# Kernel optimization log

Measured on AMD Instinct MI355X. Metric: run time of the kernel, lower is better.

The kernel has to match this reference:

```python
import jax, jax.numpy as jnp
import numpy as np
import math

D_MODEL, N_HEADS, D_FF = 512, 8, 2048
B, S = 4, 2048
EPS = 1e-6


def _layernorm(x, alpha, bias):
    # Faithful to the torch module: std is unbiased (ddof=1) and eps is added to std, not var.
    m = jnp.mean(x, axis=-1, keepdims=True)
    s = jnp.std(x, axis=-1, keepdims=True, ddof=1)
    return alpha * (x - m) / (s + EPS) + bias


def setup_inputs() -> dict:
    key = jax.random.key(0)
    ks = jax.random.split(key, 16)
    d, f = D_MODEL, D_FF
    sd = 1.0 / math.sqrt(d)
    sf = 1.0 / math.sqrt(f)
    return {
        "x": jax.random.normal(ks[0], (B, S, d), jnp.float32),
        "wq": jax.random.normal(ks[1], (d, d), jnp.float32) * sd,
        "bq": jnp.zeros((d,), jnp.float32),
        "wk": jax.random.normal(ks[2], (d, d), jnp.float32) * sd,
        "bk": jnp.zeros((d,), jnp.float32),
        "wv": jax.random.normal(ks[3], (d, d), jnp.float32) * sd,
        "bv": jnp.zeros((d,), jnp.float32),
        "wo": jax.random.normal(ks[4], (d, d), jnp.float32) * sd,
        "bo": jnp.zeros((d,), jnp.float32),
        "w1": jax.random.normal(ks[5], (d, f), jnp.float32) * sd,
        "b1": jnp.zeros((f,), jnp.float32),
        "w2": jax.random.normal(ks[6], (f, d), jnp.float32) * sf,
        "b2": jnp.zeros((d,), jnp.float32),
        "ln1_a": jnp.ones((d,), jnp.float32),
        "ln1_b": jnp.zeros((d,), jnp.float32),
        "ln2_a": jnp.ones((d,), jnp.float32),
        "ln2_b": jnp.zeros((d,), jnp.float32),
    }


def reference(x, wq, bq, wk, bk, wv, bv, wo, bo, w1, b1, w2, b2, ln1_a, ln1_b, ln2_a, ln2_b):
    b, s, d = x.shape
    h, dk = N_HEADS, d // N_HEADS
    # QKV projections -> [b, h, s, dk]
    q = (x @ wq + bq).reshape(b, s, h, dk).transpose(0, 2, 1, 3)
    k = (x @ wk + bk).reshape(b, s, h, dk).transpose(0, 2, 1, 3)
    v = (x @ wv + bv).reshape(b, s, h, dk).transpose(0, 2, 1, 3)
    # Manual scaled-dot-product attention (no mask in EncoderBlock path)
    scores = jnp.einsum("bhqd,bhkd->bhqk", q, k) / jnp.sqrt(jnp.float32(dk))
    probs = jax.nn.softmax(scores, axis=-1)
    attn = jnp.einsum("bhqk,bhkd->bhqd", probs, v)
    concat = attn.transpose(0, 2, 1, 3).reshape(b, s, d)
    mha_out = concat @ wo + bo
    # Residual + LayerNorm 1
    y = _layernorm(x + mha_out, ln1_a, ln1_b)
    # FFN + Residual + LayerNorm 2
    ff = jax.nn.relu(y @ w1 + b1) @ w2 + b2
    return _layernorm(y + ff, ln2_a, ln2_b)
```

## Files before the change

kernel.cpp:

```cpp
#include <hip/hip_runtime.h>
#include <hip/hip_bf16.h>


typedef __bf16 bf16;
typedef __bf16 bf16x4 __attribute__((ext_vector_type(4)));
typedef __bf16 bf16x8 __attribute__((ext_vector_type(8)));
typedef float  f32x4  __attribute__((ext_vector_type(4)));

#define NBATCH 4
#define SEQ    2048
#define DMODEL 512
#define NHEADS 8
#define DHEAD  64
#define DFF    2048
#define MTOT   (NBATCH * SEQ)
#define WS_NEED 73940992u

__device__ __forceinline__ f32x4 mfma16(bf16x8 a, bf16x8 b, f32x4 c) {
    return __builtin_amdgcn_mfma_f32_16x16x32_bf16(a, b, c, 0, 0, 0);
}

__device__ __forceinline__ void lds16(const bf16* g, bf16* l) {
    __builtin_amdgcn_global_load_lds(
        (const __attribute__((address_space(1))) void*)g,
        (__attribute__((address_space(3))) void*)l, 16, 0, 0);
}

__device__ __forceinline__ float scrub(float f) {
    return (fabsf(f) < 1e30f) ? f : 0.f;
}

__global__ void sentinel_kernel(bf16* out) {
    out[threadIdx.x] = (bf16)1000.0f;
}

__global__ __launch_bounds__(256) void prep_kernel(
        const float* x,
        const float* wq, const float* wk, const float* wv, const float* wo,
        const float* w1, const float* w2,
        const float* bq, const float* bk, const float* bv, const float* bo,
        const float* b1, const float* b2,
        const float* l1a, const float* l1b, const float* l2a, const float* l2b,
        bf16* __restrict__ xcv,
        bf16* __restrict__ wT, bf16* __restrict__ w1T, bf16* __restrict__ w2T,
        bf16* __restrict__ prm) {
    __shared__ bf16 tile[32][33];
    int b = blockIdx.x;
    if (b < 4096) {
        int i = (b * 256 + threadIdx.x) * 4;
        float4 f = *(const float4*)(x + i);
        bf16x4 o = {(bf16)scrub(f.x), (bf16)scrub(f.y),
                    (bf16)scrub(f.z), (bf16)scrub(f.w)};
        *(bf16x4*)(xcv + i) = o;
        return;
    }
    if (b < 4106) {
        int pb = b - 4096;
        const float* srcs[10] = {bq, bk, bv, bo, b1, b2, l1a, l1b, l2a, l2b};
        const int len[10] = {512,512,512,512,2048,512,512,512,512,512};
        const int dst[10] = {0,512,1024,1536,2048,4096,4608,5120,5632,6144};
        const float* s = srcs[pb];
        bf16* d = prm + dst[pb];
        for (int i = threadIdx.x; i < len[pb]; i += 256)
            d[i] = (bf16)scrub(s[i]);
        return;
    }
    const float* in; bf16* out; int K, N, bx, by;
    if (b < 5130) {
        int idx = b - 4106, z = idx >> 8, rem = idx & 255;
        const float* srcs[4] = {wq, wk, wv, wo};
        in = srcs[z]; out = wT + (size_t)z * 262144;
        K = 512; N = 512; bx = rem & 15; by = rem >> 4;
    } else if (b < 6154) {
        int idx = b - 5130;
        in = w1; out = w1T; K = 512; N = 2048; bx = idx & 63; by = idx >> 6;
    } else {
        int idx = b - 6154;
        in = w2; out = w2T; K = 2048; N = 512; bx = idx & 15; by = idx >> 4;
    }
    int tx = threadIdx.x & 31, ty = threadIdx.x >> 5;
    int n0 = bx * 32, k0 = by * 32;
#pragma unroll
    for (int i = 0; i < 4; i++) {
        int kl = ty * 4 + i;
        tile[kl][tx] = (bf16)scrub(in[(size_t)(k0 + kl) * N + n0 + tx]);
    }
    __syncthreads();
#pragma unroll
    for (int i = 0; i < 4; i++) {
        int nl = ty * 4 + i;
        out[(size_t)(n0 + nl) * K + k0 + tx] = tile[tx][nl];
    }
}

template <bool RELU>
__global__ __launch_bounds__(256) void gemm_bt(
        const bf16* __restrict__ A, const bf16* __restrict__ BT,
        const bf16* __restrict__ bias, bf16* __restrict__ Cout,
        int M, int N, int K) {
    constexpr int BM = 128, BN = 128, BK = 32;
    __shared__ __align__(16) bf16 As[BM * BK];
    __shared__ __align__(16) bf16 Bs[BN * BK];

    int tid  = threadIdx.x;
    int wid  = tid >> 6, lane = tid & 63;
    int quad = lane >> 4, l15 = lane & 15;
    int mb = blockIdx.x * BM, nb = blockIdx.y * BN;
    int wm = (wid >> 1) * 64, wn = (wid & 1) * 64;

    f32x4 acc[4][4] = {};

    int c0 = wid * 128 + lane, c1 = c0 + 64;
    int ar0 = c0 >> 2, ac0 = (c0 & 3) * 8;
    int ar1 = c1 >> 2, ac1 = (c1 & 3) * 8;
    bf16* lA0 = &As[(wid * 2 + 0) * 512];
    bf16* lA1 = &As[(wid * 2 + 1) * 512];
    bf16* lB0 = &Bs[(wid * 2 + 0) * 512];
    bf16* lB1 = &Bs[(wid * 2 + 1) * 512];

    for (int k0 = 0; k0 < K; k0 += BK) {
        __syncthreads();
        lds16(&A [(size_t)(mb + ar0) * K + k0 + ac0], lA0);
        lds16(&A [(size_t)(mb + ar1) * K + k0 + ac1], lA1);
        lds16(&BT[(size_t)(nb + ar0) * K + k0 + ac0], lB0);
        lds16(&BT[(size_t)(nb + ar1) * K + k0 + ac1], lB1);
        __syncthreads();

        bf16x8 af[4], bfr[4];
#pragma unroll
        for (int i = 0; i < 4; i++)
            af[i] = *(const bf16x8*)&As[(wm + i * 16 + l15) * 32 + quad * 8];
#pragma unroll
        for (int j = 0; j < 4; j++)
            bfr[j] = *(const bf16x8*)&Bs[(wn + j * 16 + l15) * 32 + quad * 8];
#pragma unroll
        for (int i = 0; i < 4; i++)
#pragma unroll
            for (int j = 0; j < 4; j++)
                acc[i][j] = mfma16(af[i], bfr[j], acc[i][j]);
    }

#pragma unroll
    for (int j = 0; j < 4; j++) {
        int n = nb + wn + j * 16 + l15;
        float bv = (float)bias[n];
#pragma unroll
        for (int i = 0; i < 4; i++) {
            int mBase = mb + wm + i * 16 + quad * 4;
#pragma unroll
            for (int r = 0; r < 4; r++) {
                float v = acc[i][j][r] + bv;
                if (RELU) v = v > 0.f ? v : 0.f;
                Cout[(size_t)(mBase + r) * N + n] = (bf16)v;
            }
        }
    }
}

template <bool RELU>
__global__ __launch_bounds__(256) void gemm_bt64(
        const bf16* __restrict__ A, const bf16* __restrict__ BT,
        const bf16* __restrict__ bias, bf16* __restrict__ Cout,
        int M, int N, int K) {
    constexpr int BM = 64, BN = 128;
    __shared__ __align__(16) bf16 As0[BM * 32], As1[BM * 32];
    __shared__ __align__(16) bf16 Bs0[BN * 32], Bs1[BN * 32];

    int tid  = threadIdx.x;
    int wid  = tid >> 6, lane = tid & 63;
    int quad = lane >> 4, l15 = lane & 15;
    int mb = blockIdx.x * BM, nb = blockIdx.y * BN;
    int wm = (wid >> 1) * 32, wn = (wid & 1) * 64;

    f32x4 acc[2][4] = {};

    int cA = wid * 64 + lane;
    int arA = cA >> 2, acA = (cA & 3) * 8;
    int cB0 = wid * 128 + lane, cB1 = cB0 + 64;
    int br0 = cB0 >> 2, bc0 = (cB0 & 3) * 8;
    int br1 = cB1 >> 2, bc1 = (cB1 & 3) * 8;
    bf16* lA0  = &As0[wid * 512];
    bf16* lA1  = &As1[wid * 512];
    bf16* lB00 = &Bs0[wid * 1024];
    bf16* lB01 = &Bs0[wid * 1024 + 512];
    bf16* lB10 = &Bs1[wid * 1024];
    bf16* lB11 = &Bs1[wid * 1024 + 512];

    for (int k0 = 0; k0 < K; k0 += 64) {
        __syncthreads();
        lds16(&A [(size_t)(mb + arA) * K + k0 + acA],      lA0);
        lds16(&A [(size_t)(mb + arA) * K + k0 + 32 + acA], lA1);
        lds16(&BT[(size_t)(nb + br0) * K + k0 + bc0],      lB00);
        lds16(&BT[(size_t)(nb + br1) * K + k0 + bc1],      lB01);
        lds16(&BT[(size_t)(nb + br0) * K + k0 + 32 + bc0], lB10);
        lds16(&BT[(size_t)(nb + br1) * K + k0 + 32 + bc1], lB11);
        __syncthreads();

        bf16x8 a0[2], a1[2], b0[4], b1[4];
#pragma unroll
        for (int i = 0; i < 2; i++) {
            a0[i] = *(const bf16x8*)&As0[(wm + i * 16 + l15) * 32 + quad * 8];
            a1[i] = *(const bf16x8*)&As1[(wm + i * 16 + l15) * 32 + quad * 8];
        }
#pragma unroll
        for (int j = 0; j < 4; j++) {
            b0[j] = *(const bf16x8*)&Bs0[(wn + j * 16 + l15) * 32 + quad * 8];
            b1[j] = *(const bf16x8*)&Bs1[(wn + j * 16 + l15) * 32 + quad * 8];
        }
#pragma unroll
        for (int i = 0; i < 2; i++)
#pragma unroll
            for (int j = 0; j < 4; j++)
                acc[i][j] = mfma16(a1[i], b1[j], mfma16(a0[i], b0[j], acc[i][j]));
    }

#pragma unroll
    for (int j = 0; j < 4; j++) {
        int n = nb + wn + j * 16 + l15;
        float bv = (float)bias[n];
#pragma unroll
        for (int i = 0; i < 2; i++) {
            int mBase = mb + wm + i * 16 + quad * 4;
#pragma unroll
            for (int r = 0; r < 4; r++) {
                float v = acc[i][j][r] + bv;
                if (RELU) v = v > 0.f ? v : 0.f;
                Cout[(size_t)(mBase + r) * N + n] = (bf16)v;
            }
        }
    }
}

__global__ __launch_bounds__(256) void gemm_qkv(
        const bf16* __restrict__ A, const bf16* __restrict__ BT,
        const bf16* __restrict__ bias,
        bf16* __restrict__ Cq, bf16* __restrict__ Ck, bf16* __restrict__ Cv,
        int M, int N, int K) {
    constexpr int BM = 128, BN = 128, BK = 32;
    __shared__ __align__(16) bf16 As[BM * BK];
    __shared__ __align__(16) bf16 Bs[BN * BK];
    __shared__ __align__(16) bf16 Ts[128 * 136];

    int tid  = threadIdx.x;
    int wid  = tid >> 6, lane = tid & 63;
    int quad = lane >> 4, l15 = lane & 15;
    int mb = blockIdx.x * BM, nb = blockIdx.y * BN;
    int wm = (wid >> 1) * 64, wn = (wid & 1) * 64;

    f32x4 acc[4][4] = {};

    int c0 = wid * 128 + lane, c1 = c0 + 64;
    int ar0 = c0 >> 2, ac0 = (c0 & 3) * 8;
    int ar1 = c1 >> 2, ac1 = (c1 & 3) * 8;
    bf16* lA0 = &As[(wid * 2 + 0) * 512];
    bf16* lA1 = &As[(wid * 2 + 1) * 512];
    bf16* lB0 = &Bs[(wid * 2 + 0) * 512];
    bf16* lB1 = &Bs[(wid * 2 + 1) * 512];

    for (int k0 = 0; k0 < K; k0 += BK) {
        __syncthreads();
        lds16(&A [(size_t)(mb + ar0) * K + k0 + ac0], lA0);
        lds16(&A [(size_t)(mb + ar1) * K + k0 + ac1], lA1);
        lds16(&BT[(size_t)(nb + ar0) * K + k0 + ac0], lB0);
        lds16(&BT[(size_t)(nb + ar1) * K + k0 + ac1], lB1);
        __syncthreads();

        bf16x8 af[4], bfr[4];
#pragma unroll
        for (int i = 0; i < 4; i++)
            af[i] = *(const bf16x8*)&As[(wm + i * 16 + l15) * 32 + quad * 8];
#pragma unroll
        for (int j = 0; j < 4; j++)
            bfr[j] = *(const bf16x8*)&Bs[(wn + j * 16 + l15) * 32 + quad * 8];
#pragma unroll
        for (int i = 0; i < 4; i++)
#pragma unroll
            for (int j = 0; j < 4; j++)
                acc[i][j] = mfma16(af[i], bfr[j], acc[i][j]);
    }

    int reg = nb >> 9;
    if (reg < 2) {
        bf16* C = reg ? Ck : Cq;
        float scl = reg ? 1.0f : 0.125f;
#pragma unroll
        for (int j = 0; j < 4; j++) {
            int n = nb + wn + j * 16 + l15;
            float bv = (float)bias[n];
            int nn = n & 511;
            int h = nn >> 6, dk = nn & 63;
#pragma unroll
            for (int i = 0; i < 4; i++) {
                int mBase = mb + wm + i * 16 + quad * 4;
#pragma unroll
                for (int r = 0; r < 4; r++) {
                    float v = (acc[i][j][r] + bv) * scl;
                    int m = mBase + r;
                    int b = m >> 11, s = m & (SEQ - 1);
                    C[((size_t)(b * NHEADS + h) * SEQ + s) * DHEAD + dk] = (bf16)v;
                }
            }
        }
    } else {
#pragma unroll
        for (int j = 0; j < 4; j++) {
            int nl = wn + j * 16 + l15;
            float bv = (float)bias[nb + nl];
#pragma unroll
            for (int i = 0; i < 4; i++) {
                int ml = wm + i * 16 + quad * 4;
                bf16x4 pk;
#pragma unroll
                for (int r = 0; r < 4; r++) pk[r] = (bf16)(acc[i][j][r] + bv);
                *(bf16x4*)&Ts[nl * 136 + ml] = pk;
            }
        }
        __syncthreads();
        int nl = tid >> 1, half = tid & 1;
        int nn = (nb + nl) & 511;
        int h = nn >> 6, dk = nn & 63;
        int bb = mb >> 11, s0 = mb & (SEQ - 1);
        bf16* dst = &Cv[((size_t)(bb * NHEADS + h) * DHEAD + dk) * SEQ + s0 + half * 64];
        const bf16* srcl = &Ts[nl * 136 + half * 64];
#pragma unroll
        for (int v = 0; v < 8; v++)
            *(uint4*)(dst + v * 8) = *(const uint4*)(srcl + v * 8);
    }
}

__global__ __launch_bounds__(256) void attn_kernel(
        const bf16* __restrict__ Q, const bf16* __restrict__ K,
        const bf16* __restrict__ VT,
        float* __restrict__ Opart, float* __restrict__ lpart) {
    __shared__ __align__(16) bf16 Ks[2][64 * 72];
    __shared__ __align__(16) bf16 Vs[2][64 * 72];
    __shared__ __align__(16) bf16 Pb[4][16 * 72];
    int tid  = threadIdx.x;
    int wid  = tid >> 6, lane = tid & 63;
    int quad = lane >> 4, l15 = lane & 15;
    int bh = blockIdx.y;
    int z  = blockIdx.z;
    int qb = blockIdx.x * 128 + wid * 32;
    int kb0 = z * (SEQ / 2);

    const bf16* Qh = Q  + (size_t)bh * SEQ * DHEAD;
    const bf16* Kh = K  + (size_t)bh * SEQ * DHEAD;
    const bf16* Vh = VT + (size_t)bh * DHEAD * SEQ;

    bf16x8 bQ0[2], bQ1[2];
#pragma unroll
    for (int c = 0; c < 2; c++) {
        const bf16* qp = &Qh[(qb + c * 16 + l15) * DHEAD + quad * 8];
        bQ0[c] = *(const bf16x8*)qp;
        bQ1[c] = *(const bf16x8*)(qp + 32);
    }

    int cc0 = tid * 2, cc1 = cc0 + 1;
    int kr0 = cc0 >> 3, kc0 = (cc0 & 7) * 8;
    int kr1 = cc1 >> 3, kc1 = (cc1 & 7) * 8;

    float lrow[2] = {0.f, 0.f};
    f32x4 Oacc[2][4] = {};

    {
        uint4 ka0 = *(const uint4*)&Kh[(size_t)(kb0 + kr0) * DHEAD + kc0];
        uint4 ka1 = *(const uint4*)&Kh[(size_t)(kb0 + kr1) * DHEAD + kc1];
        uint4 va0 = *(const uint4*)&Vh[(size_t)kr0 * SEQ + kb0 + kc0];
        uint4 va1 = *(const uint4*)&Vh[(size_t)kr1 * SEQ + kb0 + kc1];
        *(uint4*)&Ks[0][kr0 * 72 + kc0] = ka0;
        *(uint4*)&Ks[0][kr1 * 72 + kc1] = ka1;
        *(uint4*)&Vs[0][kr0 * 72 + kc0] = va0;
        *(uint4*)&Vs[0][kr1 * 72 + kc1] = va1;
    }
    __syncthreads();

    for (int it = 0; it < 16; it++) {
        int cur = it & 1, nxt = cur ^ 1;
        int kb = kb0 + (it + 1) * 64;
        uint4 nk0, nk1, nv0, nv1;
        bool pf = (it + 1 < 16);
        if (pf) {
            nk0 = *(const uint4*)&Kh[(size_t)(kb + kr0) * DHEAD + kc0];
            nk1 = *(const uint4*)&Kh[(size_t)(kb + kr1) * DHEAD + kc1];
            nv0 = *(const uint4*)&Vh[(size_t)kr0 * SEQ + kb + kc0];
            nv1 = *(const uint4*)&Vh[(size_t)kr1 * SEQ + kb + kc1];
        }

        bf16x8 aK0[4], aK1[4], bV0[4], bV1[4];
#pragma unroll
        for (int t = 0; t < 4; t++) {
            const bf16* kp = &Ks[cur][(t * 16 + l15) * 72 + quad * 8];
            aK0[t] = *(const bf16x8*)kp;
            aK1[t] = *(const bf16x8*)(kp + 32);
            const bf16* vp = &Vs[cur][(t * 16 + l15) * 72 + quad * 8];
            bV0[t] = *(const bf16x8*)vp;
            bV1[t] = *(const bf16x8*)(vp + 32);
        }

#pragma unroll
        for (int c = 0; c < 2; c++) {
            f32x4 st[4];
#pragma unroll
            for (int t = 0; t < 4; t++) {
                f32x4 zv = {0.f, 0.f, 0.f, 0.f};
                st[t] = mfma16(aK1[t], bQ1[c], mfma16(aK0[t], bQ0[c], zv));
            }
            bf16* myP = Pb[wid];
#pragma unroll
            for (int t = 0; t < 4; t++) {
                bf16x4 pk;
                float ps = 0.f;
#pragma unroll
                for (int r = 0; r < 4; r++) {
                    float p = __expf(fminf(st[t][r], 60.f));
                    ps += p;
                    pk[r] = (bf16)p;
                }
                lrow[c] += ps;
                *(bf16x4*)&myP[l15 * 72 + t * 16 + quad * 4] = pk;
            }
            bf16x8 aP0 = *(const bf16x8*)&myP[l15 * 72 + quad * 8];
            bf16x8 aP1 = *(const bf16x8*)&myP[l15 * 72 + 32 + quad * 8];
#pragma unroll
            for (int nt = 0; nt < 4; nt++)
                Oacc[c][nt] = mfma16(aP1, bV1[nt],
                                     mfma16(aP0, bV0[nt], Oacc[c][nt]));
        }

        if (pf) {
            *(uint4*)&Ks[nxt][kr0 * 72 + kc0] = nk0;
            *(uint4*)&Ks[nxt][kr1 * 72 + kc1] = nk1;
            *(uint4*)&Vs[nxt][kr0 * 72 + kc0] = nv0;
            *(uint4*)&Vs[nxt][kr1 * 72 + kc1] = nv1;
        }
        __syncthreads();
    }

    int b = bh >> 3, hd = bh & 7;
    float* Op = Opart + (size_t)z * (MTOT * (size_t)DMODEL);
#pragma unroll
    for (int c = 0; c < 2; c++) {
        float l = lrow[c];
        l += __shfl_xor(l, 16);
        l += __shfl_xor(l, 32);
        if (quad == 0)
            lpart[z * 65536 + bh * SEQ + qb + c * 16 + l15] = l;
#pragma unroll
        for (int nt = 0; nt < 4; nt++)
#pragma unroll
            for (int r = 0; r < 4; r++) {
                int s = qb + c * 16 + quad * 4 + r;
                Op[((size_t)(b * SEQ + s)) * DMODEL + hd * 64 + nt * 16 + l15]
                    = Oacc[c][nt][r];
            }
    }
}

__global__ __launch_bounds__(256) void merge_o(
        const float* __restrict__ Opart, const float* __restrict__ lpart,
        bf16* __restrict__ Out) {
    int idx4 = blockIdx.x * 256 + threadIdx.x;
    int e = idx4 * 4;
    int sg = e >> 9, col = e & 511;
    int b = sg >> 11, s = sg & (SEQ - 1), hd = col >> 6;
    int li = (b * NHEADS + hd) * SEQ + s;
    float linv = 1.f / (lpart[li] + lpart[65536 + li]);
    f32x4 o0 = ((const f32x4*)Opart)[idx4];
    f32x4 o1 = ((const f32x4*)(Opart + (size_t)MTOT * DMODEL))[idx4];
    bf16x4 o;
#pragma unroll
    for (int r = 0; r < 4; r++) o[r] = (bf16)((o0[r] + o1[r]) * linv);
    *(bf16x4*)(Out + e) = o;
}

__global__ __launch_bounds__(256) void ln_kernel(
        const bf16* __restrict__ X, const bf16* __restrict__ T,
        const bf16* __restrict__ Al, const bf16* __restrict__ Bl,
        void* __restrict__ Out, int final_out) {
    int wid = threadIdx.x >> 6, lane = threadIdx.x & 63;
    int row = blockIdx.x * 4 + wid;
    const bf16* xr = X + (size_t)row * DMODEL;
    const bf16* tr = T + (size_t)row * DMODEL;
    bf16x8 xv = *(const bf16x8*)&xr[lane * 8];
    bf16x8 tv = *(const bf16x8*)&tr[lane * 8];
    float v[8];
#pragma unroll
    for (int i = 0; i < 8; i++) v[i] = (float)xv[i] + (float)tv[i];
    float sum = 0.f, sq = 0.f;
#pragma unroll
    for (int i = 0; i < 8; i++) { sum += v[i]; sq += v[i] * v[i]; }
#pragma unroll
    for (int m = 1; m < 64; m <<= 1) {
        sum += __shfl_xor(sum, m);
        sq  += __shfl_xor(sq,  m);
    }
    float mean = sum * (1.f / DMODEL);
    float var  = (sq - DMODEL * mean * mean) * (1.f / (DMODEL - 1));
    var = var > 0.f ? var : 0.f;
    float inv = 1.f / (sqrtf(var) + 1e-6f);
#pragma unroll
    for (int i = 0; i < 8; i++) {
        int c = lane * 8 + i;
        float yv = (float)Al[c] * (v[i] - mean) * inv + (float)Bl[c];
        yv = fminf(fmaxf(yv, -1e4f), 1e4f);
        size_t idx = (size_t)row * DMODEL + c;
        if (final_out) ((float*)Out)[idx] = yv;
        else           ((bf16*)Out)[idx]  = (bf16)yv;
    }
}

extern "C" void kernel_launch(void* const* d_in, const int* in_sizes, int n_in,
                              void* d_out, int out_size, void* d_ws, size_t ws_size,
                              hipStream_t stream) {
    if (ws_size < WS_NEED) {
        sentinel_kernel<<<1, 64, 0, stream>>>((bf16*)d_out);
        return;
    }

    const float* x  = (const float*)d_in[0];
    const float* wq = (const float*)d_in[1],  *bq = (const float*)d_in[2];
    const float* wk = (const float*)d_in[3],  *bk = (const float*)d_in[4];
    const float* wv = (const float*)d_in[5],  *bv = (const float*)d_in[6];
    const float* wo = (const float*)d_in[7],  *bo = (const float*)d_in[8];
    const float* w1 = (const float*)d_in[9],  *b1 = (const float*)d_in[10];
    const float* w2 = (const float*)d_in[11], *b2 = (const float*)d_in[12];
    const float* ln1a = (const float*)d_in[13], *ln1b = (const float*)d_in[14];
    const float* ln2a = (const float*)d_in[15], *ln2b = (const float*)d_in[16];

    char* ws = (char*)d_ws;
    bf16* wT   = (bf16*)(ws + 0);
    bf16* woT  = (bf16*)(ws + 1572864);
    bf16* w1T  = (bf16*)(ws + 2097152);
    bf16* w2T  = (bf16*)(ws + 4194304);
    bf16* xcv  = (bf16*)(ws + 6291456);
    bf16* prm  = (bf16*)(ws + 14680064);
    bf16* regA = (bf16*)(ws + 14696448);
    bf16* regB = (bf16*)(ws + 23085056);
    bf16* regC = (bf16*)(ws + 31473664);
    bf16* ff1  = (bf16*)(ws + 39862272);
    float* Opart = (float*)(ws + 39862272);
    float* lpart = (float*)(ws + 73416704);
    bf16* aout = (bf16*)d_out;

    bf16 *pbq = prm, *pbo = prm + 1536;
    bf16 *pb1 = prm + 2048, *pb2 = prm + 4096;
    bf16 *pl1a = prm + 4608, *pl1b = prm + 5120;
    bf16 *pl2a = prm + 5632, *pl2b = prm + 6144;

    prep_kernel<<<7178, 256, 0, stream>>>(x, wq, wk, wv, wo, w1, w2,
                                          bq, bk, bv, bo, b1, b2,
                                          ln1a, ln1b, ln2a, ln2b,
                                          xcv, wT, w1T, w2T, prm);

    gemm_qkv<<<dim3(64, 12), 256, 0, stream>>>(xcv, wT, pbq,
                                               regA, regB, regC,
                                               MTOT, 3 * DMODEL, DMODEL);

    attn_kernel<<<dim3(SEQ / 128, NBATCH * NHEADS, 2), 256, 0, stream>>>(
        regA, regB, regC, Opart, lpart);
    merge_o<<<4096, 256, 0, stream>>>(Opart, lpart, aout);

    gemm_bt64<false><<<dim3(128, 4), 256, 0, stream>>>(aout, woT, pbo, regA,
                                                       MTOT, DMODEL, DMODEL);

    ln_kernel<<<MTOT / 4, 256, 0, stream>>>(xcv, regA, pl1a, pl1b, regB, 0);

    gemm_bt<true ><<<dim3(64, 16), 256, 0, stream>>>(regB, w1T, pb1, ff1,
                                                     MTOT, DFF, DMODEL);
    gemm_bt64<false><<<dim3(128, 4), 256, 0, stream>>>(ff1, w2T, pb2, regA,
                                                       MTOT, DMODEL, DFF);

    ln_kernel<<<MTOT / 4, 256, 0, stream>>>(regB, regA, pl2a, pl2b, d_out, 1);
}
```

Before: 294.1 us.

## Drop split-K attention merge, fold log2e into Q scale, widen GEMM K-step

Attention no longer splits the key range in two with fp32 partial outputs and a separate merge kernel. Each block now walks the full sequence and normalizes its output in-register, which removes the fp32 Opart/lpart traffic and one launch but halves the attention grid. The log2(e) factor is folded into the Q scale so the softmax can use exp2f. The 128x128 GEMMs (qkv and ffn1) now stage K=64 per barrier pair using two LDS buffers, which doubles LDS use but halves the number of synchronizations.

```diff
diff --git a/kernel.cpp b/kernel.cpp
--- a/kernel.cpp
+++ b/kernel.cpp
@@ -14,7 +14,8 @@
 #define DHEAD  64
 #define DFF    2048
 #define MTOT   (NBATCH * SEQ)
-#define WS_NEED 73940992u
+#define WS_NEED 73416704u
+#define QSCALE (0.125f * 1.44269504f)
 
 __device__ __forceinline__ f32x4 mfma16(bf16x8 a, bf16x8 b, f32x4 c) {
     return __builtin_amdgcn_mfma_f32_16x16x32_bf16(a, b, c, 0, 0, 0);
@@ -98,9 +99,9 @@
         const bf16* __restrict__ A, const bf16* __restrict__ BT,
         const bf16* __restrict__ bias, bf16* __restrict__ Cout,
         int M, int N, int K) {
-    constexpr int BM = 128, BN = 128, BK = 32;
-    __shared__ __align__(16) bf16 As[BM * BK];
-    __shared__ __align__(16) bf16 Bs[BN * BK];
+    constexpr int BM = 128, BN = 128;
+    __shared__ __align__(16) bf16 As0[BM * 32], As1[BM * 32];
+    __shared__ __align__(16) bf16 Bs0[BN * 32], Bs1[BN * 32];
 
     int tid  = threadIdx.x;
     int wid  = tid >> 6, lane = tid & 63;
@@ -113,26 +114,38 @@
     int c0 = wid * 128 + lane, c1 = c0 + 64;
     int ar0 = c0 >> 2, ac0 = (c0 & 3) * 8;
     int ar1 = c1 >> 2, ac1 = (c1 & 3) * 8;
-    bf16* lA0 = &As[(wid * 2 + 0) * 512];
-    bf16* lA1 = &As[(wid * 2 + 1) * 512];
-    bf16* lB0 = &Bs[(wid * 2 + 0) * 512];
-    bf16* lB1 = &Bs[(wid * 2 + 1) * 512];
-
-    for (int k0 = 0; k0 < K; k0 += BK) {
-        __syncthreads();
-        lds16(&A [(size_t)(mb + ar0) * K + k0 + ac0], lA0);
-        lds16(&A [(size_t)(mb + ar1) * K + k0 + ac1], lA1);
-        lds16(&BT[(size_t)(nb + ar0) * K + k0 + ac0], lB0);
-        lds16(&BT[(size_t)(nb + ar1) * K + k0 + ac1], lB1);
+    int o0 = wid * 1024, o1 = wid * 1024 + 512;
+
+    for (int k0 = 0; k0 < K; k0 += 64) {
+        __syncthreads();
+        lds16(&A [(size_t)(mb + ar0) * K + k0 + ac0],      &As0[o0]);
+        lds16(&A [(size_t)(mb + ar1) * K + k0 + ac1],      &As0[o1]);
+        lds16(&A [(size_t)(mb + ar0) * K + k0 + 32 + ac0], &As1[o0]);
+        lds16(&A [(size_t)(mb + ar1) * K + k0 + 32 + ac1], &As1[o1]);
+        lds16(&BT[(size_t)(nb + ar0) * K + k0 + ac0],      &Bs0[o0]);
+        lds16(&BT[(size_t)(nb + ar1) * K + k0 + ac1],      &Bs0[o1]);
+        lds16(&BT[(size_t)(nb + ar0) * K + k0 + 32 + ac0], &Bs1[o0]);
+        lds16(&BT[(size_t)(nb + ar1) * K + k0 + 32 + ac1], &Bs1[o1]);
         __syncthreads();
 
         bf16x8 af[4], bfr[4];
 #pragma unroll
         for (int i = 0; i < 4; i++)
-            af[i] = *(const bf16x8*)&As[(wm + i * 16 + l15) * 32 + quad * 8];
+            af[i] = *(const bf16x8*)&As0[(wm + i * 16 + l15) * 32 + quad * 8];
 #pragma unroll
         for (int j = 0; j < 4; j++)
-            bfr[j] = *(const bf16x8*)&Bs[(wn + j * 16 + l15) * 32 + quad * 8];
+            bfr[j] = *(const bf16x8*)&Bs0[(wn + j * 16 + l15) * 32 + quad * 8];
+#pragma unroll
+        for (int i = 0; i < 4; i++)
+#pragma unroll
+            for (int j = 0; j < 4; j++)
+                acc[i][j] = mfma16(af[i], bfr[j], acc[i][j]);
+#pragma unroll
+        for (int i = 0; i < 4; i++)
+            af[i] = *(const bf16x8*)&As1[(wm + i * 16 + l15) * 32 + quad * 8];
+#pragma unroll
+        for (int j = 0; j < 4; j++)
+            bfr[j] = *(const bf16x8*)&Bs1[(wn + j * 16 + l15) * 32 + quad * 8];
 #pragma unroll
         for (int i = 0; i < 4; i++)
 #pragma unroll
@@ -179,21 +192,15 @@
     int cB0 = wid * 128 + lane, cB1 = cB0 + 64;
     int br0 = cB0 >> 2, bc0 = (cB0 & 3) * 8;
     int br1 = cB1 >> 2, bc1 = (cB1 & 3) * 8;
-    bf16* lA0  = &As0[wid * 512];
-    bf16* lA1  = &As1[wid * 512];
-    bf16* lB00 = &Bs0[wid * 1024];
-    bf16* lB01 = &Bs0[wid * 1024 + 512];
-    bf16* lB10 = &Bs1[wid * 1024];
-    bf16* lB11 = &Bs1[wid * 1024 + 512];
 
     for (int k0 = 0; k0 < K; k0 += 64) {
         __syncthreads();
-        lds16(&A [(size_t)(mb + arA) * K + k0 + acA],      lA0);
-        lds16(&A [(size_t)(mb + arA) * K + k0 + 32 + acA], lA1);
-        lds16(&BT[(size_t)(nb + br0) * K + k0 + bc0],      lB00);
-        lds16(&BT[(size_t)(nb + br1) * K + k0 + bc1],      lB01);
-        lds16(&BT[(size_t)(nb + br0) * K + k0 + 32 + bc0], lB10);
-        lds16(&BT[(size_t)(nb + br1) * K + k0 + 32 + bc1], lB11);
+        lds16(&A [(size_t)(mb + arA) * K + k0 + acA],      &As0[wid * 512]);
+        lds16(&A [(size_t)(mb + arA) * K + k0 + 32 + acA], &As1[wid * 512]);
+        lds16(&BT[(size_t)(nb + br0) * K + k0 + bc0],      &Bs0[wid * 1024]);
+        lds16(&BT[(size_t)(nb + br1) * K + k0 + bc1],      &Bs0[wid * 1024 + 512]);
+        lds16(&BT[(size_t)(nb + br0) * K + k0 + 32 + bc0], &Bs1[wid * 1024]);
+        lds16(&BT[(size_t)(nb + br1) * K + k0 + 32 + bc1], &Bs1[wid * 1024 + 512]);
         __syncthreads();
 
         bf16x8 a0[2], a1[2], b0[4], b1[4];
@@ -236,9 +243,9 @@
         const bf16* __restrict__ bias,
         bf16* __restrict__ Cq, bf16* __restrict__ Ck, bf16* __restrict__ Cv,
         int M, int N, int K) {
-    constexpr int BM = 128, BN = 128, BK = 32;
-    __shared__ __align__(16) bf16 As[BM * BK];
-    __shared__ __align__(16) bf16 Bs[BN * BK];
+    constexpr int BM = 128, BN = 128;
+    __shared__ __align__(16) bf16 As0[BM * 32], As1[BM * 32];
+    __shared__ __align__(16) bf16 Bs0[BN * 32], Bs1[BN * 32];
     __shared__ __align__(16) bf16 Ts[128 * 136];
 
     int tid  = threadIdx.x;
@@ -252,26 +259,38 @@
     int c0 = wid * 128 + lane, c1 = c0 + 64;
     int ar0 = c0 >> 2, ac0 = (c0 & 3) * 8;
     int ar1 = c1 >> 2, ac1 = (c1 & 3) * 8;
-    bf16* lA0 = &As[(wid * 2 + 0) * 512];
-    bf16* lA1 = &As[(wid * 2 + 1) * 512];
-    bf16* lB0 = &Bs[(wid * 2 + 0) * 512];
-    bf16* lB1 = &Bs[(wid * 2 + 1) * 512];
-
-    for (int k0 = 0; k0 < K; k0 += BK) {
-        __syncthreads();
-        lds16(&A [(size_t)(mb + ar0) * K + k0 + ac0], lA0);
-        lds16(&A [(size_t)(mb + ar1) * K + k0 + ac1], lA1);
-        lds16(&BT[(size_t)(nb + ar0) * K + k0 + ac0], lB0);
-        lds16(&BT[(size_t)(nb + ar1) * K + k0 + ac1], lB1);
+    int o0 = wid * 1024, o1 = wid * 1024 + 512;
+
+    for (int k0 = 0; k0 < K; k0 += 64) {
+        __syncthreads();
+        lds16(&A [(size_t)(mb + ar0) * K + k0 + ac0],      &As0[o0]);
+        lds16(&A [(size_t)(mb + ar1) * K + k0 + ac1],      &As0[o1]);
+        lds16(&A [(size_t)(mb + ar0) * K + k0 + 32 + ac0], &As1[o0]);
+        lds16(&A [(size_t)(mb + ar1) * K + k0 + 32 + ac1], &As1[o1]);
+        lds16(&BT[(size_t)(nb + ar0) * K + k0 + ac0],      &Bs0[o0]);
+        lds16(&BT[(size_t)(nb + ar1) * K + k0 + ac1],      &Bs0[o1]);
+        lds16(&BT[(size_t)(nb + ar0) * K + k0 + 32 + ac0], &Bs1[o0]);
+        lds16(&BT[(size_t)(nb + ar1) * K + k0 + 32 + ac1], &Bs1[o1]);
         __syncthreads();
 
         bf16x8 af[4], bfr[4];
 #pragma unroll
         for (int i = 0; i < 4; i++)
-            af[i] = *(const bf16x8*)&As[(wm + i * 16 + l15) * 32 + quad * 8];
+            af[i] = *(const bf16x8*)&As0[(wm + i * 16 + l15) * 32 + quad * 8];
 #pragma unroll
         for (int j = 0; j < 4; j++)
-            bfr[j] = *(const bf16x8*)&Bs[(wn + j * 16 + l15) * 32 + quad * 8];
+            bfr[j] = *(const bf16x8*)&Bs0[(wn + j * 16 + l15) * 32 + quad * 8];
+#pragma unroll
+        for (int i = 0; i < 4; i++)
+#pragma unroll
+            for (int j = 0; j < 4; j++)
+                acc[i][j] = mfma16(af[i], bfr[j], acc[i][j]);
+#pragma unroll
+        for (int i = 0; i < 4; i++)
+            af[i] = *(const bf16x8*)&As1[(wm + i * 16 + l15) * 32 + quad * 8];
+#pragma unroll
+        for (int j = 0; j < 4; j++)
+            bfr[j] = *(const bf16x8*)&Bs1[(wn + j * 16 + l15) * 32 + quad * 8];
 #pragma unroll
         for (int i = 0; i < 4; i++)
 #pragma unroll
@@ -282,7 +301,7 @@
     int reg = nb >> 9;
     if (reg < 2) {
         bf16* C = reg ? Ck : Cq;
-        float scl = reg ? 1.0f : 0.125f;
+        float scl = reg ? 1.0f : QSCALE;
 #pragma unroll
         for (int j = 0; j < 4; j++) {
             int n = nb + wn + j * 16 + l15;
@@ -330,8 +349,7 @@
 
 __global__ __launch_bounds__(256) void attn_kernel(
         const bf16* __restrict__ Q, const bf16* __restrict__ K,
-        const bf16* __restrict__ VT,
-        float* __restrict__ Opart, float* __restrict__ lpart) {
+        const bf16* __restrict__ VT, bf16* __restrict__ Out) {
     __shared__ __align__(16) bf16 Ks[2][64 * 72];
     __shared__ __align__(16) bf16 Vs[2][64 * 72];
     __shared__ __align__(16) bf16 Pb[4][16 * 72];
@@ -339,9 +357,7 @@
     int wid  = tid >> 6, lane = tid & 63;
     int quad = lane >> 4, l15 = lane & 15;
     int bh = blockIdx.y;
-    int z  = blockIdx.z;
     int qb = blockIdx.x * 128 + wid * 32;
-    int kb0 = z * (SEQ / 2);
 
     const bf16* Qh = Q  + (size_t)bh * SEQ * DHEAD;
     const bf16* Kh = K  + (size_t)bh * SEQ * DHEAD;
@@ -363,10 +379,10 @@
     f32x4 Oacc[2][4] = {};
 
     {
-        uint4 ka0 = *(const uint4*)&Kh[(size_t)(kb0 + kr0) * DHEAD + kc0];
-        uint4 ka1 = *(const uint4*)&Kh[(size_t)(kb0 + kr1) * DHEAD + kc1];
-        uint4 va0 = *(const uint4*)&Vh[(size_t)kr0 * SEQ + kb0 + kc0];
-        uint4 va1 = *(const uint4*)&Vh[(size_t)kr1 * SEQ + kb0 + kc1];
+        uint4 ka0 = *(const uint4*)&Kh[(size_t)kr0 * DHEAD + kc0];
+        uint4 ka1 = *(const uint4*)&Kh[(size_t)kr1 * DHEAD + kc1];
+        uint4 va0 = *(const uint4*)&Vh[(size_t)kr0 * SEQ + kc0];
+        uint4 va1 = *(const uint4*)&Vh[(size_t)kr1 * SEQ + kc1];
         *(uint4*)&Ks[0][kr0 * 72 + kc0] = ka0;
         *(uint4*)&Ks[0][kr1 * 72 + kc1] = ka1;
         *(uint4*)&Vs[0][kr0 * 72 + kc0] = va0;
@@ -374,11 +390,11 @@
     }
     __syncthreads();
 
-    for (int it = 0; it < 16; it++) {
+    for (int it = 0; it < SEQ / 64; it++) {
         int cur = it & 1, nxt = cur ^ 1;
-        int kb = kb0 + (it + 1) * 64;
+        int kb = (it + 1) * 64;
         uint4 nk0, nk1, nv0, nv1;
-        bool pf = (it + 1 < 16);
+        bool pf = (it + 1 < SEQ / 64);
         if (pf) {
             nk0 = *(const uint4*)&Kh[(size_t)(kb + kr0) * DHEAD + kc0];
             nk1 = *(const uint4*)&Kh[(size_t)(kb + kr1) * DHEAD + kc1];
@@ -412,7 +428,7 @@
                 float ps = 0.f;
 #pragma unroll
                 for (int r = 0; r < 4; r++) {
-                    float p = __expf(fminf(st[t][r], 60.f));
+                    float p = exp2f(fminf(st[t][r], 60.f));
                     ps += p;
                     pk[r] = (bf16)p;
                 }
@@ -437,40 +453,24 @@
     }
 
     int b = bh >> 3, hd = bh & 7;
-    float* Op = Opart + (size_t)z * (MTOT * (size_t)DMODEL);
 #pragma unroll
     for (int c = 0; c < 2; c++) {
         float l = lrow[c];
         l += __shfl_xor(l, 16);
         l += __shfl_xor(l, 32);
-        if (quad == 0)
-            lpart[z * 65536 + bh * SEQ + qb + c * 16 + l15] = l;
+        float linv[4];
+#pragma unroll
+        for (int r = 0; r < 4; r++)
+            linv[r] = 1.f / __shfl(l, quad * 4 + r);
 #pragma unroll
         for (int nt = 0; nt < 4; nt++)
 #pragma unroll
             for (int r = 0; r < 4; r++) {
                 int s = qb + c * 16 + quad * 4 + r;
-                Op[((size_t)(b * SEQ + s)) * DMODEL + hd * 64 + nt * 16 + l15]
-                    = Oacc[c][nt][r];
-            }
-    }
-}
-
-__global__ __launch_bounds__(256) void merge_o(
-        const float* __restrict__ Opart, const float* __restrict__ lpart,
-        bf16* __restrict__ Out) {
-    int idx4 = blockIdx.x * 256 + threadIdx.x;
-    int e = idx4 * 4;
-    int sg = e >> 9, col = e & 511;
-    int b = sg >> 11, s = sg & (SEQ - 1), hd = col >> 6;
-    int li = (b * NHEADS + hd) * SEQ + s;
-    float linv = 1.f / (lpart[li] + lpart[65536 + li]);
-    f32x4 o0 = ((const f32x4*)Opart)[idx4];
-    f32x4 o1 = ((const f32x4*)(Opart + (size_t)MTOT * DMODEL))[idx4];
-    bf16x4 o;
-#pragma unroll
-    for (int r = 0; r < 4; r++) o[r] = (bf16)((o0[r] + o1[r]) * linv);
-    *(bf16x4*)(Out + e) = o;
+                Out[((size_t)(b * SEQ + s)) * DMODEL + hd * 64 + nt * 16 + l15]
+                    = (bf16)(Oacc[c][nt][r] * linv[r]);
+            }
+    }
 }
 
 __global__ __launch_bounds__(256) void ln_kernel(
@@ -538,8 +538,6 @@
     bf16* regB = (bf16*)(ws + 23085056);
     bf16* regC = (bf16*)(ws + 31473664);
     bf16* ff1  = (bf16*)(ws + 39862272);
-    float* Opart = (float*)(ws + 39862272);
-    float* lpart = (float*)(ws + 73416704);
     bf16* aout = (bf16*)d_out;
 
     bf16 *pbq = prm, *pbo = prm + 1536;
@@ -556,9 +554,8 @@
                                                regA, regB, regC,
                                                MTOT, 3 * DMODEL, DMODEL);
 
-    attn_kernel<<<dim3(SEQ / 128, NBATCH * NHEADS, 2), 256, 0, stream>>>(
-        regA, regB, regC, Opart, lpart);
-    merge_o<<<4096, 256, 0, stream>>>(Opart, lpart, aout);
+    attn_kernel<<<dim3(SEQ / 128, NBATCH * NHEADS), 256, 0, stream>>>(
+        regA, regB, regC, aout);
 
     gemm_bt64<false><<<dim3(128, 4), 256, 0, stream>>>(aout, woT, pbo, regA,
                                                        MTOT, DMODEL, DMODEL);
```

New measurement: 307.0 us. 4.4% more time.
